# Performance work log

Measured on AMD Instinct MI355X. Metric: run time of the kernel, lower is better.

The kernel has to match this reference:

```python
import jax, jax.numpy as jnp
import numpy as np

NEG_SLOPE = 0.2  # PyG GATConv default LeakyReLU negative slope
NUM_GRAPHS = 256


def gat_conv(x, edge_src, edge_dst, W, att_src, att_dst, bias):
    """PyG-style GATConv. x:[N,Fin], W:[H*C,Fin], att_*:[H,C], bias:[H*C]."""
    N = x.shape[0]
    H, C = att_src.shape
    h = (x @ W.T).reshape(N, H, C)                       # [N,H,C]
    a_src = jnp.sum(h * att_src, axis=-1)                # [N,H]
    a_dst = jnp.sum(h * att_dst, axis=-1)                # [N,H]
    e = jax.nn.leaky_relu(a_src[edge_src] + a_dst[edge_dst], NEG_SLOPE)  # [E,H]
    # segment softmax over edges sharing the same destination node
    m = jax.ops.segment_max(e, edge_dst, num_segments=N)
    ex = jnp.exp(e - m[edge_dst])
    den = jax.ops.segment_sum(ex, edge_dst, num_segments=N)
    alpha = ex / (den[edge_dst] + 1e-16)                 # [E,H]
    out = jax.ops.segment_sum(h[edge_src] * alpha[..., None], edge_dst,
                              num_segments=N)            # [N,H,C]
    return out.reshape(N, H * C) + bias


def setup_inputs() -> dict:
    key = jax.random.key(0)
    ks = jax.random.split(key, 16)
    N, E, Fin = 20000, 320000, 128
    H1, C1 = 8, 64          # conv1: heads=8, hidden_dim1=64 -> concat 512
    D1 = H1 * C1            # 512
    D2 = 128                # hidden_dim2, conv2 heads=1
    OUT = 2
    s = lambda k, shp, fan: jax.random.normal(k, shp, jnp.float32) * (1.0 / np.sqrt(fan))
    x = jax.random.normal(ks[0], (N, Fin), jnp.float32)
    edge_index = jax.random.randint(ks[1], (2, E), 0, N, jnp.int32)
    batch = jnp.sort(jax.random.randint(ks[2], (N,), 0, NUM_GRAPHS, jnp.int32))
    return {
        "x": x, "edge_index": edge_index, "batch": batch,
        "W1": s(ks[3], (D1, Fin), Fin), "att_src1": s(ks[4], (H1, C1), C1),
        "att_dst1": s(ks[5], (H1, C1), C1), "b1": jnp.zeros((D1,), jnp.float32),
        "W2": s(ks[6], (D2, D1), D1), "att_src2": s(ks[7], (1, D2), D2),
        "att_dst2": s(ks[8], (1, D2), D2), "b2": jnp.zeros((D2,), jnp.float32),
        "w_attn": s(ks[9], (D2, 1), D2), "b_attn": jnp.zeros((1,), jnp.float32),
        "w_mask": s(ks[10], (D2, 1), D2), "b_mask": jnp.zeros((1,), jnp.float32),
        "W_out": s(ks[11], (OUT, D2), D2), "b_out": jnp.zeros((OUT,), jnp.float32),
    }


def reference(x, edge_index, batch, W1, att_src1, att_dst1, b1,
              W2, att_src2, att_dst2, b2, w_attn, b_attn, w_mask, b_mask,
              W_out, b_out):
    N = x.shape[0]
    loops = jnp.arange(N, dtype=edge_index.dtype)
    src = jnp.concatenate([edge_index[0], loops])  # PyG add_self_loops=True
    dst = jnp.concatenate([edge_index[1], loops])

    h = gat_conv(x, src, dst, W1, att_src1, att_dst1, b1)   # [N, 512]
    h = jax.nn.relu(h)                                      # dropout = identity (eval)
    h = gat_conv(h, src, dst, W2, att_src2, att_dst2, b2)   # [N, 128]
    h = jax.nn.relu(h)

    # attention pooling over graphs in the batch
    attn_scores = h @ w_attn + b_attn                       # [N,1]
    node_mask = jax.nn.sigmoid(h @ w_mask + b_mask)         # [N,1]
    weighted = h * (attn_scores * node_mask)                # [N,128]
    pooled = jax.ops.segment_sum(weighted, batch, num_segments=NUM_GRAPHS)
    return pooled @ W_out.T + b_out                         # [256, 2]
```

## Files before the change

kernel.cpp:

```cpp
#include <hip/hip_runtime.h>
#include <math.h>


#define NEG_SLOPE 0.2f

using bf16x8 = __attribute__((ext_vector_type(8))) __bf16;
using f32x4  = __attribute__((ext_vector_type(4))) float;

__device__ __forceinline__ ushort f2bf(float f) {
    unsigned u = __float_as_uint(f);
    unsigned r = (u + 0x7FFFu + ((u >> 16) & 1u)) >> 16;
    return (ushort)r;
}
__device__ __forceinline__ unsigned pack2(float a, float b) {
    return (unsigned)f2bf(a) | ((unsigned)f2bf(b) << 16);
}
__device__ __forceinline__ void unpack8(uint4 u, float* f) {
    f[0] = __uint_as_float(u.x << 16); f[1] = __uint_as_float(u.x & 0xFFFF0000u);
    f[2] = __uint_as_float(u.y << 16); f[3] = __uint_as_float(u.y & 0xFFFF0000u);
    f[4] = __uint_as_float(u.z << 16); f[5] = __uint_as_float(u.z & 0xFFFF0000u);
    f[6] = __uint_as_float(u.w << 16); f[7] = __uint_as_float(u.w & 0xFFFF0000u);
}
__device__ __forceinline__ void unpack4(uint2 u, float* f) {
    f[0] = __uint_as_float(u.x << 16); f[1] = __uint_as_float(u.x & 0xFFFF0000u);
    f[2] = __uint_as_float(u.y << 16); f[3] = __uint_as_float(u.y & 0xFFFF0000u);
}

__global__ __launch_bounds__(256) void cvt_bf16(const float* __restrict__ in,
                                                ushort* __restrict__ out, int n4) {
    int i = blockIdx.x * 256 + threadIdx.x;
    if (i >= n4) return;
    float4 v = ((const float4*)in)[i];
    uint2 o;
    o.x = pack2(v.x, v.y);
    o.y = pack2(v.z, v.w);
    ((uint2*)out)[i] = o;
}

#define LDSB 40
__global__ __launch_bounds__(256) void gemm_mfma(const ushort* __restrict__ A,
                                                 const ushort* __restrict__ B,
                                                 ushort* __restrict__ C,
                                                 int M, int N, int K) {
    __shared__ ushort As[128 * LDSB];
    __shared__ ushort Bs[128 * LDSB];
    int t = threadIdx.x;
    int wave = t >> 6, lane = t & 63;
    int quad = lane >> 4, l16 = lane & 15;
    int m0 = blockIdx.x * 128;
    int n0 = blockIdx.y * 128;
    int wm = (wave & 1) * 64;
    int wn = (wave >> 1) * 64;
    int srow = t >> 1;
    int sseg = (t & 1) * 16;
    f32x4 acc[4][4] = {};
    for (int k0 = 0; k0 < K; k0 += 32) {
        uint4 av0, av1, bv0, bv1;
        {
            int grow = m0 + srow;
            if (grow < M) {
                const uint4* gp = (const uint4*)(A + (size_t)grow * K + k0 + sseg);
                av0 = gp[0]; av1 = gp[1];
            } else {
                av0 = make_uint4(0, 0, 0, 0); av1 = av0;
            }
            const uint4* gq = (const uint4*)(B + (size_t)(n0 + srow) * K + k0 + sseg);
            bv0 = gq[0]; bv1 = gq[1];
        }
        __syncthreads();
        *(uint4*)&As[srow * LDSB + sseg]     = av0;
        *(uint4*)&As[srow * LDSB + sseg + 8] = av1;
        *(uint4*)&Bs[srow * LDSB + sseg]     = bv0;
        *(uint4*)&Bs[srow * LDSB + sseg + 8] = bv1;
        __syncthreads();
        bf16x8 af[4], bf[4];
#pragma unroll
        for (int i = 0; i < 4; ++i)
            af[i] = *(const bf16x8*)&As[(wm + i * 16 + l16) * LDSB + quad * 8];
#pragma unroll
        for (int j = 0; j < 4; ++j)
            bf[j] = *(const bf16x8*)&Bs[(wn + j * 16 + l16) * LDSB + quad * 8];
#pragma unroll
        for (int i = 0; i < 4; ++i)
#pragma unroll
            for (int j = 0; j < 4; ++j)
                acc[i][j] = __builtin_amdgcn_mfma_f32_16x16x32_bf16(
                    af[i], bf[j], acc[i][j], 0, 0, 0);
    }
#pragma unroll
    for (int i = 0; i < 4; ++i) {
#pragma unroll
        for (int r = 0; r < 4; ++r) {
            int grow = m0 + wm + i * 16 + quad * 4 + r;
            if (grow < M) {
#pragma unroll
                for (int j = 0; j < 4; ++j) {
                    int gcol = n0 + wn + j * 16 + l16;
                    C[(size_t)grow * N + gcol] = f2bf(acc[i][j][r]);
                }
            }
        }
    }
}

__global__ __launch_bounds__(256) void scores1(const ushort* __restrict__ h1,
                                               const float* __restrict__ att_s,
                                               const float* __restrict__ att_d,
                                               float* __restrict__ a1s,
                                               float* __restrict__ a1d, int N) {
    int node = blockIdx.x * 4 + (threadIdx.x >> 6);
    if (node >= N) return;
    int lane = threadIdx.x & 63;
    uint4 u = *(const uint4*)(h1 + (size_t)node * 512 + lane * 8);
    float h[8];
    unpack8(u, h);
    const float4* sp = (const float4*)(att_s + lane * 8);
    const float4* dp = (const float4*)(att_d + lane * 8);
    float4 s0 = sp[0], s1 = sp[1], d0 = dp[0], d1 = dp[1];
    float ps = h[0] * s0.x + h[1] * s0.y + h[2] * s0.z + h[3] * s0.w +
               h[4] * s1.x + h[5] * s1.y + h[6] * s1.z + h[7] * s1.w;
    float pd = h[0] * d0.x + h[1] * d0.y + h[2] * d0.z + h[3] * d0.w +
               h[4] * d1.x + h[5] * d1.y + h[6] * d1.z + h[7] * d1.w;
#pragma unroll
    for (int off = 1; off < 8; off <<= 1) {
        ps += __shfl_xor(ps, off);
        pd += __shfl_xor(pd, off);
    }
    if ((lane & 7) == 0) {
        a1s[node * 8 + (lane >> 3)] = ps;
        a1d[node * 8 + (lane >> 3)] = pd;
    }
}

__global__ void count_edges(const int* __restrict__ dst, int* cnt, int E) {
    int e = blockIdx.x * 256 + threadIdx.x;
    if (e < E) atomicAdd(&cnt[dst[e]], 1);
}

__global__ __launch_bounds__(1024) void scan_offsets(const int* cnt, int* row_start,
                                                     int* cursor, int N) {
    __shared__ int sm[1024];
    int t = threadIdx.x;
    int per = (N + 1023) / 1024;
    int beg = t * per;
    int end = beg + per; if (end > N) end = N;
    int sum = 0;
    for (int i = beg; i < end; ++i) sum += cnt[i];
    sm[t] = sum;
    __syncthreads();
    for (int off = 1; off < 1024; off <<= 1) {
        int add = (t >= off) ? sm[t - off] : 0;
        __syncthreads();
        sm[t] += add;
        __syncthreads();
    }
    int run = sm[t] - sum;
    for (int i = beg; i < end; ++i) {
        int c = cnt[i];
        row_start[i] = run;
        cursor[i] = run;
        run += c;
    }
    if (t == 1023) row_start[N] = run;
}

__global__ void fill_edges(const int* __restrict__ src, const int* __restrict__ dst,
                           int* cursor, int* __restrict__ srcs, int E) {
    int e = blockIdx.x * 256 + threadIdx.x;
    if (e < E) {
        int pos = atomicAdd(&cursor[dst[e]], 1);
        srcs[pos] = src[e];
    }
}

__global__ __launch_bounds__(256) void agg1(const ushort* __restrict__ h1,
                                            const float* __restrict__ a1s,
                                            const float* __restrict__ a1d,
                                            const int* __restrict__ row_start,
                                            const int* __restrict__ srcs,
                                            const float* __restrict__ b1,
                                            ushort* __restrict__ r1, int N) {
    int node = blockIdx.x * 4 + (threadIdx.x >> 6);
    if (node >= N) return;
    int lane = threadIdx.x & 63;
    int head = lane >> 3;
    int f0 = lane * 8;
    int pbeg = row_start[node], pend = row_start[node + 1];
    float ad = a1d[node * 8 + head];
    float es = a1s[node * 8 + head] + ad;
    es = es > 0.f ? es : NEG_SLOPE * es;
    float ex_self = __expf(es);
    float den = ex_self;
    float q[8];
    unpack8(*(const uint4*)(h1 + (size_t)node * 512 + f0), q);
    float acc[8];
#pragma unroll
    for (int j = 0; j < 8; ++j) acc[j] = ex_self * q[j];
    for (int p = pbeg; p < pend; ++p) {
        int s = srcs[p];
        float e = a1s[s * 8 + head] + ad;
        e = e > 0.f ? e : NEG_SLOPE * e;
        float ex = __expf(e);
        den += ex;
        float v[8];
        unpack8(*(const uint4*)(h1 + (size_t)s * 512 + f0), v);
#pragma unroll
        for (int j = 0; j < 8; ++j) acc[j] += ex * v[j];
    }
    float rden = 1.0f / (den + 1e-16f);
    const float4* bp = (const float4*)(b1 + f0);
    float4 b0 = bp[0], b1v = bp[1];
    float o[8];
    o[0] = fmaxf(acc[0] * rden + b0.x, 0.f);
    o[1] = fmaxf(acc[1] * rden + b0.y, 0.f);
    o[2] = fmaxf(acc[2] * rden + b0.z, 0.f);
    o[3] = fmaxf(acc[3] * rden + b0.w, 0.f);
    o[4] = fmaxf(acc[4] * rden + b1v.x, 0.f);
    o[5] = fmaxf(acc[5] * rden + b1v.y, 0.f);
    o[6] = fmaxf(acc[6] * rden + b1v.z, 0.f);
    o[7] = fmaxf(acc[7] * rden + b1v.w, 0.f);
    uint4 ov;
    ov.x = pack2(o[0], o[1]); ov.y = pack2(o[2], o[3]);
    ov.z = pack2(o[4], o[5]); ov.w = pack2(o[6], o[7]);
    *(uint4*)(r1 + (size_t)node * 512 + f0) = ov;
}

__global__ __launch_bounds__(256) void scores2(const ushort* __restrict__ h2,
                                               const float* __restrict__ att_s,
                                               const float* __restrict__ att_d,
                                               float* __restrict__ a2s,
                                               float* __restrict__ a2d, int N) {
    int node = blockIdx.x * 4 + (threadIdx.x >> 6);
    if (node >= N) return;
    int lane = threadIdx.x & 63;
    unsigned u = *(const unsigned*)(h2 + (size_t)node * 128 + lane * 2);
    float h0 = __uint_as_float(u << 16), h1v = __uint_as_float(u & 0xFFFF0000u);
    float2 s = *(const float2*)(att_s + lane * 2);
    float2 d = *(const float2*)(att_d + lane * 2);
    float ps = h0 * s.x + h1v * s.y;
    float pd = h0 * d.x + h1v * d.y;
#pragma unroll
    for (int off = 1; off < 64; off <<= 1) {
        ps += __shfl_xor(ps, off);
        pd += __shfl_xor(pd, off);
    }
    if (lane == 0) { a2s[node] = ps; a2d[node] = pd; }
}

__global__ __launch_bounds__(256) void agg2(const ushort* __restrict__ h2,
                                            const float* __restrict__ a2s,
                                            const float* __restrict__ a2d,
                                            const int* __restrict__ row_start,
                                            const int* __restrict__ srcs,
                                            const float* __restrict__ b2,
                                            float* __restrict__ r2, int N) {
    int node = blockIdx.x * 8 + (threadIdx.x >> 5);
    if (node >= N) return;
    int sub = threadIdx.x & 31;
    int f0 = sub * 4;
    int pbeg = row_start[node], pend = row_start[node + 1];
    float ad = a2d[node];
    float es = a2s[node] + ad;
    es = es > 0.f ? es : NEG_SLOPE * es;
    float ex_self = __expf(es);
    float den = ex_self;
    float q[4];
    unpack4(*(const uint2*)(h2 + (size_t)node * 128 + f0), q);
    float acc[4];
#pragma unroll
    for (int j = 0; j < 4; ++j) acc[j] = ex_self * q[j];
    for (int p = pbeg; p < pend; ++p) {
        int s = srcs[p];
        float e = a2s[s] + ad;
        e = e > 0.f ? e : NEG_SLOPE * e;
        float ex = __expf(e);
        den += ex;
        float v[4];
        unpack4(*(const uint2*)(h2 + (size_t)s * 128 + f0), v);
#pragma unroll
        for (int j = 0; j < 4; ++j) acc[j] += ex * v[j];
    }
    float rden = 1.0f / (den + 1e-16f);
    float4 bv = *(const float4*)(b2 + f0);
    float4 o;
    o.x = fmaxf(acc[0] * rden + bv.x, 0.f);
    o.y = fmaxf(acc[1] * rden + bv.y, 0.f);
    o.z = fmaxf(acc[2] * rden + bv.z, 0.f);
    o.w = fmaxf(acc[3] * rden + bv.w, 0.f);
    *(float4*)(r2 + (size_t)node * 128 + f0) = o;
}

__global__ __launch_bounds__(256) void pool_kernel(const float* __restrict__ r2,
                                                   const int* __restrict__ batch,
                                                   const float* __restrict__ w_attn,
                                                   const float* __restrict__ b_attn,
                                                   const float* __restrict__ w_mask,
                                                   const float* __restrict__ b_mask,
                                                   float* pooled, int N) {
    int node = blockIdx.x * 4 + (threadIdx.x >> 6);
    if (node >= N) return;
    int lane = threadIdx.x & 63;
    float2 h = *(const float2*)(r2 + (size_t)node * 128 + lane * 2);
    float2 wa = *(const float2*)(w_attn + lane * 2);
    float2 wm = *(const float2*)(w_mask + lane * 2);
    float pa = h.x * wa.x + h.y * wa.y;
    float pm = h.x * wm.x + h.y * wm.y;
#pragma unroll
    for (int off = 1; off < 64; off <<= 1) {
        pa += __shfl_xor(pa, off);
        pm += __shfl_xor(pm, off);
    }
    float attn = pa + b_attn[0];
    float mask = 1.0f / (1.0f + __expf(-(pm + b_mask[0])));
    float w = attn * mask;
    int g = batch[node];
    atomicAdd(&pooled[g * 128 + lane * 2], h.x * w);
    atomicAdd(&pooled[g * 128 + lane * 2 + 1], h.y * w);
}

__global__ void final_kernel(const float* __restrict__ pooled,
                             const float* __restrict__ W_out,
                             const float* __restrict__ b_out,
                             float* __restrict__ out) {
    int tid = blockIdx.x * 256 + threadIdx.x;
    if (tid >= 512) return;
    int g = tid >> 1, o = tid & 1;
    const float* p = pooled + g * 128;
    const float* w = W_out + o * 128;
    float s = 0.f;
#pragma unroll 4
    for (int f = 0; f < 128; ++f) s += p[f] * w[f];
    out[tid] = s + b_out[o];
}

extern "C" void kernel_launch(void* const* d_in, const int* in_sizes, int n_in,
                              void* d_out, int out_size, void* d_ws, size_t ws_size,
                              hipStream_t stream) {
    const float* x        = (const float*)d_in[0];
    const int* edge_index = (const int*)d_in[1];
    const int* batch      = (const int*)d_in[2];
    const float* W1       = (const float*)d_in[3];
    const float* att_src1 = (const float*)d_in[4];
    const float* att_dst1 = (const float*)d_in[5];
    const float* b1       = (const float*)d_in[6];
    const float* W2       = (const float*)d_in[7];
    const float* att_src2 = (const float*)d_in[8];
    const float* att_dst2 = (const float*)d_in[9];
    const float* b2       = (const float*)d_in[10];
    const float* w_attn   = (const float*)d_in[11];
    const float* b_attn   = (const float*)d_in[12];
    const float* w_mask   = (const float*)d_in[13];
    const float* b_mask   = (const float*)d_in[14];
    const float* W_out    = (const float*)d_in[15];
    const float* b_out    = (const float*)d_in[16];
    float* out = (float*)d_out;

    int N = in_sizes[0] / 128;
    int E = in_sizes[1] / 2;
    const int* esrc = edge_index;
    const int* edst = edge_index + E;

    char* ws = (char*)d_ws;
    size_t off = 0;
    auto alloc = [&](size_t bytes) {
        void* p = ws + off;
        off = (off + bytes + 255) & ~(size_t)255;
        return p;
    };
    ushort* h1       = (ushort*)alloc((size_t)N * 512 * 2);
    ushort* r1       = (ushort*)alloc((size_t)N * 512 * 2);
    ushort* h2       = (ushort*)alloc((size_t)N * 128 * 2);
    float*  r2       = (float*)alloc((size_t)N * 128 * 4);
    ushort* xb       = (ushort*)alloc((size_t)N * 128 * 2);
    ushort* w1b      = (ushort*)alloc((size_t)512 * 128 * 2);
    ushort* w2b      = (ushort*)alloc((size_t)128 * 512 * 2);
    float*  a1s      = (float*)alloc((size_t)N * 8 * 4);
    float*  a1d      = (float*)alloc((size_t)N * 8 * 4);
    float*  a2s      = (float*)alloc((size_t)N * 4);
    float*  a2d      = (float*)alloc((size_t)N * 4);
    int*    row_start= (int*)alloc((size_t)(N + 1) * 4);
    int*    cursor   = (int*)alloc((size_t)N * 4);
    int*    srcs     = (int*)alloc((size_t)E * 4);
    float*  pooled   = (float*)alloc((size_t)256 * 128 * 4);

    hipMemsetAsync(cursor, 0, (size_t)N * 4, stream);
    hipMemsetAsync(pooled, 0, 256 * 128 * 4, stream);

    dim3 b256(256);
    int nx4 = N * 128 / 4;
    cvt_bf16<<<(nx4 + 255) / 256, b256, 0, stream>>>(x, xb, nx4);
    cvt_bf16<<<(512 * 128 / 4 + 255) / 256, b256, 0, stream>>>(W1, w1b, 512 * 128 / 4);
    cvt_bf16<<<(128 * 512 / 4 + 255) / 256, b256, 0, stream>>>(W2, w2b, 128 * 512 / 4);
    count_edges<<<(E + 255) / 256, b256, 0, stream>>>(edst, cursor, E);
    scan_offsets<<<1, 1024, 0, stream>>>(cursor, row_start, cursor, N);
    fill_edges<<<(E + 255) / 256, b256, 0, stream>>>(esrc, edst, cursor, srcs, E);
    gemm_mfma<<<dim3((N + 127) / 128, 512 / 128), b256, 0, stream>>>(xb, w1b, h1, N, 512, 128);
    scores1<<<(N + 3) / 4, b256, 0, stream>>>(h1, att_src1, att_dst1, a1s, a1d, N);
    agg1<<<(N + 3) / 4, b256, 0, stream>>>(h1, a1s, a1d, row_start, srcs, b1, r1, N);
    gemm_mfma<<<dim3((N + 127) / 128, 128 / 128), b256, 0, stream>>>(r1, w2b, h2, N, 128, 512);
    scores2<<<(N + 3) / 4, b256, 0, stream>>>(h2, att_src2, att_dst2, a2s, a2d, N);
    agg2<<<(N + 7) / 8, b256, 0, stream>>>(h2, a2s, a2d, row_start, srcs, b2, r2, N);
    pool_kernel<<<(N + 3) / 4, b256, 0, stream>>>(r2, batch, w_attn, b_attn, w_mask,
                                                  b_mask, pooled, N);
    final_kernel<<<2, b256, 0, stream>>>(pooled, W_out, b_out, out);
}
```

Baseline: 316.8 us.

## Split GAT aggregation across heads and edge halves with unrolled gathers

Both aggregation kernels are restructured so that each wavefront handles one head (or one half of the features) of a node. The two 32-lane halves of the wavefront process alternating edges and are combined with a cross-half shuffle. The edge loop is unrolled by four so several independent gather loads are in flight at once, aiming to raise memory-level parallelism on the irregular neighbour gathers. The cost is many more blocks, narrower 4-byte gathers instead of 16-byte ones, and repeated reads of row_start and the destination scores for every head.

```diff
diff --git a/kernel.cpp b/kernel.cpp
--- a/kernel.cpp
+++ b/kernel.cpp
@@ -15,16 +15,8 @@
 __device__ __forceinline__ unsigned pack2(float a, float b) {
     return (unsigned)f2bf(a) | ((unsigned)f2bf(b) << 16);
 }
-__device__ __forceinline__ void unpack8(uint4 u, float* f) {
-    f[0] = __uint_as_float(u.x << 16); f[1] = __uint_as_float(u.x & 0xFFFF0000u);
-    f[2] = __uint_as_float(u.y << 16); f[3] = __uint_as_float(u.y & 0xFFFF0000u);
-    f[4] = __uint_as_float(u.z << 16); f[5] = __uint_as_float(u.z & 0xFFFF0000u);
-    f[6] = __uint_as_float(u.w << 16); f[7] = __uint_as_float(u.w & 0xFFFF0000u);
-}
-__device__ __forceinline__ void unpack4(uint2 u, float* f) {
-    f[0] = __uint_as_float(u.x << 16); f[1] = __uint_as_float(u.x & 0xFFFF0000u);
-    f[2] = __uint_as_float(u.y << 16); f[3] = __uint_as_float(u.y & 0xFFFF0000u);
-}
+__device__ __forceinline__ float bflo(unsigned u) { return __uint_as_float(u << 16); }
+__device__ __forceinline__ float bfhi(unsigned u) { return __uint_as_float(u & 0xFFFF0000u); }
 
 __global__ __launch_bounds__(256) void cvt_bf16(const float* __restrict__ in,
                                                 ushort* __restrict__ out, int n4) {
@@ -113,7 +105,10 @@
     int lane = threadIdx.x & 63;
     uint4 u = *(const uint4*)(h1 + (size_t)node * 512 + lane * 8);
     float h[8];
-    unpack8(u, h);
+    h[0] = bflo(u.x); h[1] = bfhi(u.x);
+    h[2] = bflo(u.y); h[3] = bfhi(u.y);
+    h[4] = bflo(u.z); h[5] = bfhi(u.z);
+    h[6] = bflo(u.w); h[7] = bfhi(u.w);
     const float4* sp = (const float4*)(att_s + lane * 8);
     const float4* dp = (const float4*)(att_d + lane * 8);
     float4 s0 = sp[0], s1 = sp[1], d0 = dp[0], d1 = dp[1];
@@ -173,56 +168,73 @@
     }
 }
 
-__global__ __launch_bounds__(256) void agg1(const ushort* __restrict__ h1,
-                                            const float* __restrict__ a1s,
-                                            const float* __restrict__ a1d,
-                                            const int* __restrict__ row_start,
-                                            const int* __restrict__ srcs,
-                                            const float* __restrict__ b1,
-                                            ushort* __restrict__ r1, int N) {
-    int node = blockIdx.x * 4 + (threadIdx.x >> 6);
+__global__ __launch_bounds__(256) void agg1s(const ushort* __restrict__ h1,
+                                             const float* __restrict__ a1s,
+                                             const float* __restrict__ a1d,
+                                             const int* __restrict__ row_start,
+                                             const int* __restrict__ srcs,
+                                             const float* __restrict__ b1,
+                                             ushort* __restrict__ r1, int N) {
+    int bid = blockIdx.x;
+    int head = bid & 7;
+    int node = (bid >> 3) * 4 + (threadIdx.x >> 6);
     if (node >= N) return;
     int lane = threadIdx.x & 63;
-    int head = lane >> 3;
-    int f0 = lane * 8;
+    int sub = lane & 31;
+    int half = lane >> 5;
+    int fbase = head * 64 + sub * 2;
     int pbeg = row_start[node], pend = row_start[node + 1];
     float ad = a1d[node * 8 + head];
     float es = a1s[node * 8 + head] + ad;
     es = es > 0.f ? es : NEG_SLOPE * es;
     float ex_self = __expf(es);
-    float den = ex_self;
-    float q[8];
-    unpack8(*(const uint4*)(h1 + (size_t)node * 512 + f0), q);
-    float acc[8];
-#pragma unroll
-    for (int j = 0; j < 8; ++j) acc[j] = ex_self * q[j];
-    for (int p = pbeg; p < pend; ++p) {
+    unsigned uq = *(const unsigned*)(h1 + (size_t)node * 512 + fbase);
+    float acc0 = 0.f, acc1 = 0.f, den = 0.f;
+    int p = pbeg + half;
+    for (; p + 6 < pend; p += 8) {
+        int s0 = srcs[p];
+        int s1 = srcs[p + 2];
+        int s2 = srcs[p + 4];
+        int s3 = srcs[p + 6];
+        unsigned u0 = *(const unsigned*)(h1 + (size_t)s0 * 512 + fbase);
+        unsigned u1 = *(const unsigned*)(h1 + (size_t)s1 * 512 + fbase);
+        unsigned u2 = *(const unsigned*)(h1 + (size_t)s2 * 512 + fbase);
+        unsigned u3 = *(const unsigned*)(h1 + (size_t)s3 * 512 + fbase);
+        float as0 = a1s[s0 * 8 + head];
+        float as1 = a1s[s1 * 8 + head];
+        float as2 = a1s[s2 * 8 + head];
+        float as3 = a1s[s3 * 8 + head];
+        float e0 = as0 + ad; e0 = e0 > 0.f ? e0 : NEG_SLOPE * e0;
+        float e1 = as1 + ad; e1 = e1 > 0.f ? e1 : NEG_SLOPE * e1;
+        float e2 = as2 + ad; e2 = e2 > 0.f ? e2 : NEG_SLOPE * e2;
+        float e3 = as3 + ad; e3 = e3 > 0.f ? e3 : NEG_SLOPE * e3;
+        float x0 = __expf(e0), x1 = __expf(e1), x2 = __expf(e2), x3 = __expf(e3);
+        den += (x0 + x1) + (x2 + x3);
+        acc0 += x0 * bflo(u0); acc1 += x0 * bfhi(u0);
+        acc0 += x1 * bflo(u1); acc1 += x1 * bfhi(u1);
+        acc0 += x2 * bflo(u2); acc1 += x2 * bfhi(u2);
+        acc0 += x3 * bflo(u3); acc1 += x3 * bfhi(u3);
+    }
+    for (; p < pend; p += 2) {
         int s = srcs[p];
+        unsigned u = *(const unsigned*)(h1 + (size_t)s * 512 + fbase);
         float e = a1s[s * 8 + head] + ad;
         e = e > 0.f ? e : NEG_SLOPE * e;
         float ex = __expf(e);
         den += ex;
-        float v[8];
-        unpack8(*(const uint4*)(h1 + (size_t)s * 512 + f0), v);
-#pragma unroll
-        for (int j = 0; j < 8; ++j) acc[j] += ex * v[j];
-    }
+        acc0 += ex * bflo(u); acc1 += ex * bfhi(u);
+    }
+    acc0 += __shfl_xor(acc0, 32);
+    acc1 += __shfl_xor(acc1, 32);
+    den  += __shfl_xor(den, 32);
+    den  += ex_self;
+    acc0 += ex_self * bflo(uq);
+    acc1 += ex_self * bfhi(uq);
     float rden = 1.0f / (den + 1e-16f);
-    const float4* bp = (const float4*)(b1 + f0);
-    float4 b0 = bp[0], b1v = bp[1];
-    float o[8];
-    o[0] = fmaxf(acc[0] * rden + b0.x, 0.f);
-    o[1] = fmaxf(acc[1] * rden + b0.y, 0.f);
-    o[2] = fmaxf(acc[2] * rden + b0.z, 0.f);
-    o[3] = fmaxf(acc[3] * rden + b0.w, 0.f);
-    o[4] = fmaxf(acc[4] * rden + b1v.x, 0.f);
-    o[5] = fmaxf(acc[5] * rden + b1v.y, 0.f);
-    o[6] = fmaxf(acc[6] * rden + b1v.z, 0.f);
-    o[7] = fmaxf(acc[7] * rden + b1v.w, 0.f);
-    uint4 ov;
-    ov.x = pack2(o[0], o[1]); ov.y = pack2(o[2], o[3]);
-    ov.z = pack2(o[4], o[5]); ov.w = pack2(o[6], o[7]);
-    *(uint4*)(r1 + (size_t)node * 512 + f0) = ov;
+    float o0 = fmaxf(acc0 * rden + b1[fbase], 0.f);
+    float o1 = fmaxf(acc1 * rden + b1[fbase + 1], 0.f);
+    if (half == 0)
+        *(unsigned*)(r1 + (size_t)node * 512 + fbase) = pack2(o0, o1);
 }
 
 __global__ __launch_bounds__(256) void scores2(const ushort* __restrict__ h2,
@@ -234,7 +246,7 @@
     if (node >= N) return;
     int lane = threadIdx.x & 63;
     unsigned u = *(const unsigned*)(h2 + (size_t)node * 128 + lane * 2);
-    float h0 = __uint_as_float(u << 16), h1v = __uint_as_float(u & 0xFFFF0000u);
+    float h0 = bflo(u), h1v = bfhi(u);
     float2 s = *(const float2*)(att_s + lane * 2);
     float2 d = *(const float2*)(att_d + lane * 2);
     float ps = h0 * s.x + h1v * s.y;
@@ -247,47 +259,75 @@
     if (lane == 0) { a2s[node] = ps; a2d[node] = pd; }
 }
 
-__global__ __launch_bounds__(256) void agg2(const ushort* __restrict__ h2,
-                                            const float* __restrict__ a2s,
-                                            const float* __restrict__ a2d,
-                                            const int* __restrict__ row_start,
-                                            const int* __restrict__ srcs,
-                                            const float* __restrict__ b2,
-                                            float* __restrict__ r2, int N) {
-    int node = blockIdx.x * 8 + (threadIdx.x >> 5);
+__global__ __launch_bounds__(256) void agg2s(const ushort* __restrict__ h2,
+                                             const float* __restrict__ a2s,
+                                             const float* __restrict__ a2d,
+                                             const int* __restrict__ row_start,
+                                             const int* __restrict__ srcs,
+                                             const float* __restrict__ b2,
+                                             float* __restrict__ r2, int N) {
+    int bid = blockIdx.x;
+    int hh = bid & 1;
+    int node = (bid >> 1) * 4 + (threadIdx.x >> 6);
     if (node >= N) return;
-    int sub = threadIdx.x & 31;
-    int f0 = sub * 4;
+    int lane = threadIdx.x & 63;
+    int sub = lane & 31;
+    int half = lane >> 5;
+    int fbase = hh * 64 + sub * 2;
     int pbeg = row_start[node], pend = row_start[node + 1];
     float ad = a2d[node];
     float es = a2s[node] + ad;
     es = es > 0.f ? es : NEG_SLOPE * es;
     float ex_self = __expf(es);
-    float den = ex_self;
-    float q[4];
-    unpack4(*(const uint2*)(h2 + (size_t)node * 128 + f0), q);
-    float acc[4];
-#pragma unroll
-    for (int j = 0; j < 4; ++j) acc[j] = ex_self * q[j];
-    for (int p = pbeg; p < pend; ++p) {
+    unsigned uq = *(const unsigned*)(h2 + (size_t)node * 128 + fbase);
+    float acc0 = 0.f, acc1 = 0.f, den = 0.f;
+    int p = pbeg + half;
+    for (; p + 6 < pend; p += 8) {
+        int s0 = srcs[p];
+        int s1 = srcs[p + 2];
+        int s2 = srcs[p + 4];
+        int s3 = srcs[p + 6];
+        unsigned u0 = *(const unsigned*)(h2 + (size_t)s0 * 128 + fbase);
+        unsigned u1 = *(const unsigned*)(h2 + (size_t)s1 * 128 + fbase);
+        unsigned u2 = *(const unsigned*)(h2 + (size_t)s2 * 128 + fbase);
+        unsigned u3 = *(const unsigned*)(h2 + (size_t)s3 * 128 + fbase);
+        float as0 = a2s[s0];
+        float as1 = a2s[s1];
+        float as2 = a2s[s2];
+        float as3 = a2s[s3];
+        float e0 = as0 + ad; e0 = e0 > 0.f ? e0 : NEG_SLOPE * e0;
+        float e1 = as1 + ad; e1 = e1 > 0.f ? e1 : NEG_SLOPE * e1;
+        float e2 = as2 + ad; e2 = e2 > 0.f ? e2 : NEG_SLOPE * e2;
+        float e3 = as3 + ad; e3 = e3 > 0.f ? e3 : NEG_SLOPE * e3;
+        float x0 = __expf(e0), x1 = __expf(e1), x2 = __expf(e2), x3 = __expf(e3);
+        den += (x0 + x1) + (x2 + x3);
+        acc0 += x0 * bflo(u0); acc1 += x0 * bfhi(u0);
+        acc0 += x1 * bflo(u1); acc1 += x1 * bfhi(u1);
+        acc0 += x2 * bflo(u2); acc1 += x2 * bfhi(u2);
+        acc0 += x3 * bflo(u3); acc1 += x3 * bfhi(u3);
+    }
+    for (; p < pend; p += 2) {
         int s = srcs[p];
+        unsigned u = *(const unsigned*)(h2 + (size_t)s * 128 + fbase);
         float e = a2s[s] + ad;
         e = e > 0.f ? e : NEG_SLOPE * e;
         float ex = __expf(e);
         den += ex;
-        float v[4];
-        unpack4(*(const uint2*)(h2 + (size_t)s * 128 + f0), v);
-#pragma unroll
-        for (int j = 0; j < 4; ++j) acc[j] += ex * v[j];
-    }
+        acc0 += ex * bflo(u); acc1 += ex * bfhi(u);
+    }
+    acc0 += __shfl_xor(acc0, 32);
+    acc1 += __shfl_xor(acc1, 32);
+    den  += __shfl_xor(den, 32);
+    den  += ex_self;
+    acc0 += ex_self * bflo(uq);
+    acc1 += ex_self * bfhi(uq);
     float rden = 1.0f / (den + 1e-16f);
-    float4 bv = *(const float4*)(b2 + f0);
-    float4 o;
-    o.x = fmaxf(acc[0] * rden + bv.x, 0.f);
-    o.y = fmaxf(acc[1] * rden + bv.y, 0.f);
-    o.z = fmaxf(acc[2] * rden + bv.z, 0.f);
-    o.w = fmaxf(acc[3] * rden + bv.w, 0.f);
-    *(float4*)(r2 + (size_t)node * 128 + f0) = o;
+    float o0 = fmaxf(acc0 * rden + b2[fbase], 0.f);
+    float o1 = fmaxf(acc1 * rden + b2[fbase + 1], 0.f);
+    if (half == 0) {
+        float2 ov; ov.x = o0; ov.y = o1;
+        *(float2*)(r2 + (size_t)node * 128 + fbase) = ov;
+    }
 }
 
 __global__ __launch_bounds__(256) void pool_kernel(const float* __restrict__ r2,
@@ -396,10 +436,10 @@
     fill_edges<<<(E + 255) / 256, b256, 0, stream>>>(esrc, edst, cursor, srcs, E);
     gemm_mfma<<<dim3((N + 127) / 128, 512 / 128), b256, 0, stream>>>(xb, w1b, h1, N, 512, 128);
     scores1<<<(N + 3) / 4, b256, 0, stream>>>(h1, att_src1, att_dst1, a1s, a1d, N);
-    agg1<<<(N + 3) / 4, b256, 0, stream>>>(h1, a1s, a1d, row_start, srcs, b1, r1, N);
+    agg1s<<<((N + 3) / 4) * 8, b256, 0, stream>>>(h1, a1s, a1d, row_start, srcs, b1, r1, N);
     gemm_mfma<<<dim3((N + 127) / 128, 128 / 128), b256, 0, stream>>>(r1, w2b, h2, N, 128, 512);
     scores2<<<(N + 3) / 4, b256, 0, stream>>>(h2, att_src2, att_dst2, a2s, a2d, N);
-    agg2<<<(N + 7) / 8, b256, 0, stream>>>(h2, a2s, a2d, row_start, srcs, b2, r2, N);
+    agg2s<<<((N + 3) / 4) * 2, b256, 0, stream>>>(h2, a2s, a2d, row_start, srcs, b2, r2, N);
     pool_kernel<<<(N + 3) / 4, b256, 0, stream>>>(r2, batch, w_attn, b_attn, w_mask,
                                                   b_mask, pooled, N);
     final_kernel<<<2, b256, 0, stream>>>(pooled, W_out, b_out, out);
```

New measurement: 332.6 us. 5.0% more time.

## Parallelize GAT aggregation across edges within a wavefront, split heads across blocks

Applied to the files above, without the earlier changes.

Both aggregation kernels now process eight neighbor edges at once per wavefront: lanes are grouped into eight edge slots, each holding eight features, and partial sums and denominators are combined with xor shuffles. agg1 assigns one head per block, giving eight times more blocks, and agg2 splits its 128 features across two blocks. The goal is to raise memory-level parallelism and cut the serial per-edge latency chain of the gather loop, which averages about 16 edges per node. The cost is shuffle reductions, masked tail iterations, and repeated loads of srcs and scores across the head blocks.

```diff
diff --git a/kernel.cpp b/kernel.cpp
--- a/kernel.cpp
+++ b/kernel.cpp
@@ -15,15 +15,13 @@
 __device__ __forceinline__ unsigned pack2(float a, float b) {
     return (unsigned)f2bf(a) | ((unsigned)f2bf(b) << 16);
 }
+__device__ __forceinline__ float bflo(unsigned u) { return __uint_as_float(u << 16); }
+__device__ __forceinline__ float bfhi(unsigned u) { return __uint_as_float(u & 0xFFFF0000u); }
 __device__ __forceinline__ void unpack8(uint4 u, float* f) {
-    f[0] = __uint_as_float(u.x << 16); f[1] = __uint_as_float(u.x & 0xFFFF0000u);
-    f[2] = __uint_as_float(u.y << 16); f[3] = __uint_as_float(u.y & 0xFFFF0000u);
-    f[4] = __uint_as_float(u.z << 16); f[5] = __uint_as_float(u.z & 0xFFFF0000u);
-    f[6] = __uint_as_float(u.w << 16); f[7] = __uint_as_float(u.w & 0xFFFF0000u);
-}
-__device__ __forceinline__ void unpack4(uint2 u, float* f) {
-    f[0] = __uint_as_float(u.x << 16); f[1] = __uint_as_float(u.x & 0xFFFF0000u);
-    f[2] = __uint_as_float(u.y << 16); f[3] = __uint_as_float(u.y & 0xFFFF0000u);
+    f[0] = bflo(u.x); f[1] = bfhi(u.x);
+    f[2] = bflo(u.y); f[3] = bfhi(u.y);
+    f[4] = bflo(u.z); f[5] = bfhi(u.z);
+    f[6] = bflo(u.w); f[7] = bfhi(u.w);
 }
 
 __global__ __launch_bounds__(256) void cvt_bf16(const float* __restrict__ in,
@@ -173,56 +171,74 @@
     }
 }
 
-__global__ __launch_bounds__(256) void agg1(const ushort* __restrict__ h1,
-                                            const float* __restrict__ a1s,
-                                            const float* __restrict__ a1d,
-                                            const int* __restrict__ row_start,
-                                            const int* __restrict__ srcs,
-                                            const float* __restrict__ b1,
-                                            ushort* __restrict__ r1, int N) {
-    int node = blockIdx.x * 4 + (threadIdx.x >> 6);
+__global__ __launch_bounds__(256) void agg1g(const ushort* __restrict__ h1,
+                                             const float* __restrict__ a1s,
+                                             const float* __restrict__ a1d,
+                                             const int* __restrict__ row_start,
+                                             const int* __restrict__ srcs,
+                                             const float* __restrict__ b1,
+                                             ushort* __restrict__ r1, int N) {
+    int bid = blockIdx.x;
+    int head = bid & 7;
+    int node = (bid >> 3) * 4 + (threadIdx.x >> 6);
     if (node >= N) return;
     int lane = threadIdx.x & 63;
-    int head = lane >> 3;
-    int f0 = lane * 8;
+    int g = lane >> 3;
+    int fl = lane & 7;
+    int fbase = head * 64 + fl * 8;
     int pbeg = row_start[node], pend = row_start[node + 1];
     float ad = a1d[node * 8 + head];
+    float acc[8] = {};
+    float den = 0.f;
+    for (int p = pbeg; p < pend; p += 8) {
+        int pg = p + g;
+        bool ok = pg < pend;
+        int s = srcs[ok ? pg : pbeg];
+        uint4 u = *(const uint4*)(h1 + (size_t)s * 512 + fbase);
+        float e = a1s[s * 8 + head] + ad;
+        e = e > 0.f ? e : NEG_SLOPE * e;
+        float x = ok ? __expf(e) : 0.f;
+        den += x;
+        float v[8];
+        unpack8(u, v);
+#pragma unroll
+        for (int j = 0; j < 8; ++j) acc[j] += x * v[j];
+    }
+#pragma unroll
+    for (int j = 0; j < 8; ++j) {
+        acc[j] += __shfl_xor(acc[j], 8);
+        acc[j] += __shfl_xor(acc[j], 16);
+        acc[j] += __shfl_xor(acc[j], 32);
+    }
+    den += __shfl_xor(den, 8);
+    den += __shfl_xor(den, 16);
+    den += __shfl_xor(den, 32);
     float es = a1s[node * 8 + head] + ad;
     es = es > 0.f ? es : NEG_SLOPE * es;
     float ex_self = __expf(es);
-    float den = ex_self;
+    den += ex_self;
     float q[8];
-    unpack8(*(const uint4*)(h1 + (size_t)node * 512 + f0), q);
-    float acc[8];
-#pragma unroll
-    for (int j = 0; j < 8; ++j) acc[j] = ex_self * q[j];
-    for (int p = pbeg; p < pend; ++p) {
-        int s = srcs[p];
-        float e = a1s[s * 8 + head] + ad;
-        e = e > 0.f ? e : NEG_SLOPE * e;
-        float ex = __expf(e);
-        den += ex;
-        float v[8];
-        unpack8(*(const uint4*)(h1 + (size_t)s * 512 + f0), v);
-#pragma unroll
-        for (int j = 0; j < 8; ++j) acc[j] += ex * v[j];
-    }
-    float rden = 1.0f / (den + 1e-16f);
-    const float4* bp = (const float4*)(b1 + f0);
-    float4 b0 = bp[0], b1v = bp[1];
-    float o[8];
-    o[0] = fmaxf(acc[0] * rden + b0.x, 0.f);
-    o[1] = fmaxf(acc[1] * rden + b0.y, 0.f);
-    o[2] = fmaxf(acc[2] * rden + b0.z, 0.f);
-    o[3] = fmaxf(acc[3] * rden + b0.w, 0.f);
-    o[4] = fmaxf(acc[4] * rden + b1v.x, 0.f);
-    o[5] = fmaxf(acc[5] * rden + b1v.y, 0.f);
-    o[6] = fmaxf(acc[6] * rden + b1v.z, 0.f);
-    o[7] = fmaxf(acc[7] * rden + b1v.w, 0.f);
-    uint4 ov;
-    ov.x = pack2(o[0], o[1]); ov.y = pack2(o[2], o[3]);
-    ov.z = pack2(o[4], o[5]); ov.w = pack2(o[6], o[7]);
-    *(uint4*)(r1 + (size_t)node * 512 + f0) = ov;
+    unpack8(*(const uint4*)(h1 + (size_t)node * 512 + fbase), q);
+#pragma unroll
+    for (int j = 0; j < 8; ++j) acc[j] += ex_self * q[j];
+    if (g == 0) {
+        float rden = 1.0f / (den + 1e-16f);
+        const float4* bp = (const float4*)(b1 + fbase);
+        float4 b0 = bp[0], b1v = bp[1];
+        float o[8];
+        o[0] = fmaxf(acc[0] * rden + b0.x, 0.f);
+        o[1] = fmaxf(acc[1] * rden + b0.y, 0.f);
+        o[2] = fmaxf(acc[2] * rden + b0.z, 0.f);
+        o[3] = fmaxf(acc[3] * rden + b0.w, 0.f);
+        o[4] = fmaxf(acc[4] * rden + b1v.x, 0.f);
+        o[5] = fmaxf(acc[5] * rden + b1v.y, 0.f);
+        o[6] = fmaxf(acc[6] * rden + b1v.z, 0.f);
+        o[7] = fmaxf(acc[7] * rden + b1v.w, 0.f);
+        uint4 ov;
+        ov.x = pack2(o[0], o[1]); ov.y = pack2(o[2], o[3]);
+        ov.z = pack2(o[4], o[5]); ov.w = pack2(o[6], o[7]);
+        *(uint4*)(r1 + (size_t)node * 512 + fbase) = ov;
+    }
 }
 
 __global__ __launch_bounds__(256) void scores2(const ushort* __restrict__ h2,
@@ -234,7 +250,7 @@
     if (node >= N) return;
     int lane = threadIdx.x & 63;
     unsigned u = *(const unsigned*)(h2 + (size_t)node * 128 + lane * 2);
-    float h0 = __uint_as_float(u << 16), h1v = __uint_as_float(u & 0xFFFF0000u);
+    float h0 = bflo(u), h1v = bfhi(u);
     float2 s = *(const float2*)(att_s + lane * 2);
     float2 d = *(const float2*)(att_d + lane * 2);
     float ps = h0 * s.x + h1v * s.y;
@@ -247,47 +263,72 @@
     if (lane == 0) { a2s[node] = ps; a2d[node] = pd; }
 }
 
-__global__ __launch_bounds__(256) void agg2(const ushort* __restrict__ h2,
-                                            const float* __restrict__ a2s,
-                                            const float* __restrict__ a2d,
-                                            const int* __restrict__ row_start,
-                                            const int* __restrict__ srcs,
-                                            const float* __restrict__ b2,
-                                            float* __restrict__ r2, int N) {
-    int node = blockIdx.x * 8 + (threadIdx.x >> 5);
+__global__ __launch_bounds__(256) void agg2g(const ushort* __restrict__ h2,
+                                             const float* __restrict__ a2s,
+                                             const float* __restrict__ a2d,
+                                             const int* __restrict__ row_start,
+                                             const int* __restrict__ srcs,
+                                             const float* __restrict__ b2,
+                                             float* __restrict__ r2, int N) {
+    int bid = blockIdx.x;
+    int hh = bid & 1;
+    int node = (bid >> 1) * 4 + (threadIdx.x >> 6);
     if (node >= N) return;
-    int sub = threadIdx.x & 31;
-    int f0 = sub * 4;
+    int lane = threadIdx.x & 63;
+    int g = lane >> 3;
+    int fl = lane & 7;
+    int fbase = hh * 64 + fl * 8;
     int pbeg = row_start[node], pend = row_start[node + 1];
     float ad = a2d[node];
+    float acc[8] = {};
+    float den = 0.f;
+    for (int p = pbeg; p < pend; p += 8) {
+        int pg = p + g;
+        bool ok = pg < pend;
+        int s = srcs[ok ? pg : pbeg];
+        uint4 u = *(const uint4*)(h2 + (size_t)s * 128 + fbase);
+        float e = a2s[s] + ad;
+        e = e > 0.f ? e : NEG_SLOPE * e;
+        float x = ok ? __expf(e) : 0.f;
+        den += x;
+        float v[8];
+        unpack8(u, v);
+#pragma unroll
+        for (int j = 0; j < 8; ++j) acc[j] += x * v[j];
+    }
+#pragma unroll
+    for (int j = 0; j < 8; ++j) {
+        acc[j] += __shfl_xor(acc[j], 8);
+        acc[j] += __shfl_xor(acc[j], 16);
+        acc[j] += __shfl_xor(acc[j], 32);
+    }
+    den += __shfl_xor(den, 8);
+    den += __shfl_xor(den, 16);
+    den += __shfl_xor(den, 32);
     float es = a2s[node] + ad;
     es = es > 0.f ? es : NEG_SLOPE * es;
     float ex_self = __expf(es);
-    float den = ex_self;
-    float q[4];
-    unpack4(*(const uint2*)(h2 + (size_t)node * 128 + f0), q);
-    float acc[4];
-#pragma unroll
-    for (int j = 0; j < 4; ++j) acc[j] = ex_self * q[j];
-    for (int p = pbeg; p < pend; ++p) {
-        int s = srcs[p];
-        float e = a2s[s] + ad;
-        e = e > 0.f ? e : NEG_SLOPE * e;
-        float ex = __expf(e);
-        den += ex;
-        float v[4];
-        unpack4(*(const uint2*)(h2 + (size_t)s * 128 + f0), v);
-#pragma unroll
-        for (int j = 0; j < 4; ++j) acc[j] += ex * v[j];
-    }
-    float rden = 1.0f / (den + 1e-16f);
-    float4 bv = *(const float4*)(b2 + f0);
-    float4 o;
-    o.x = fmaxf(acc[0] * rden + bv.x, 0.f);
-    o.y = fmaxf(acc[1] * rden + bv.y, 0.f);
-    o.z = fmaxf(acc[2] * rden + bv.z, 0.f);
-    o.w = fmaxf(acc[3] * rden + bv.w, 0.f);
-    *(float4*)(r2 + (size_t)node * 128 + f0) = o;
+    den += ex_self;
+    float q[8];
+    unpack8(*(const uint4*)(h2 + (size_t)node * 128 + fbase), q);
+#pragma unroll
+    for (int j = 0; j < 8; ++j) acc[j] += ex_self * q[j];
+    if (g == 0) {
+        float rden = 1.0f / (den + 1e-16f);
+        const float4* bp = (const float4*)(b2 + fbase);
+        float4 b0 = bp[0], b1v = bp[1];
+        float4 o0, o1;
+        o0.x = fmaxf(acc[0] * rden + b0.x, 0.f);
+        o0.y = fmaxf(acc[1] * rden + b0.y, 0.f);
+        o0.z = fmaxf(acc[2] * rden + b0.z, 0.f);
+        o0.w = fmaxf(acc[3] * rden + b0.w, 0.f);
+        o1.x = fmaxf(acc[4] * rden + b1v.x, 0.f);
+        o1.y = fmaxf(acc[5] * rden + b1v.y, 0.f);
+        o1.z = fmaxf(acc[6] * rden + b1v.z, 0.f);
+        o1.w = fmaxf(acc[7] * rden + b1v.w, 0.f);
+        *(float4*)(r2 + (size_t)node * 128 + fbase) = o0;
+        *(float4*)(r2 + (size_t)node * 128 + fbase + 4) = o1;
+    }
 }
 
 __global__ __launch_bounds__(256) void pool_kernel(const float* __restrict__ r2,
@@ -396,10 +437,10 @@
     fill_edges<<<(E + 255) / 256, b256, 0, stream>>>(esrc, edst, cursor, srcs, E);
     gemm_mfma<<<dim3((N + 127) / 128, 512 / 128), b256, 0, stream>>>(xb, w1b, h1, N, 512, 128);
     scores1<<<(N + 3) / 4, b256, 0, stream>>>(h1, att_src1, att_dst1, a1s, a1d, N);
-    agg1<<<(N + 3) / 4, b256, 0, stream>>>(h1, a1s, a1d, row_start, srcs, b1, r1, N);
+    agg1g<<<((N + 3) / 4) * 8, b256, 0, stream>>>(h1, a1s, a1d, row_start, srcs, b1, r1, N);
     gemm_mfma<<<dim3((N + 127) / 128, 128 / 128), b256, 0, stream>>>(r1, w2b, h2, N, 128, 512);
     scores2<<<(N + 3) / 4, b256, 0, stream>>>(h2, att_src2, att_dst2, a2s, a2d, N);
-    agg2<<<(N + 7) / 8, b256, 0, stream>>>(h2, a2s, a2d, row_start, srcs, b2, r2, N);
+    agg2g<<<((N + 3) / 4) * 2, b256, 0, stream>>>(h2, a2s, a2d, row_start, srcs, b2, r2, N);
     pool_kernel<<<(N + 3) / 4, b256, 0, stream>>>(r2, batch, w_attn, b_attn, w_mask,
                                                   b_mask, pooled, N);
     final_kernel<<<2, b256, 0, stream>>>(pooled, W_out, b_out, out);
```

New measurement: 325.8 us. 1.03x slower.
